# Kernel tuning notes

Measured on AMD Instinct MI355X. Metric: run time of the kernel, lower is better.

## Reference

```python
import jax, jax.numpy as jnp
import numpy as np

IMG = 1024
P0, P1 = 32, 16          # patch_size = [32, 16], P0 = 2*P1 required by stride-2 conv
C = 1                    # num_channels (must be 1 for unflatten(encoded, 1) to be valid)
N0 = (IMG // P0) ** 2    # 1024 patches at coarse scale
N1 = (IMG // P1) ** 2    # 4096 patches at fine scale
D0 = C * P0 * P0         # 1024 projection dim (coarse)
D1 = C * P1 * P1         # 256 projection dim (fine)
B = 8
BN_EPS = 1e-3            # keras BatchNormalization default
LRELU_ALPHA = 0.3        # keras LeakyReLU default


def setup_inputs() -> dict:
    key = jax.random.key(0)
    ks = jax.random.split(key, 9)
    return {
        "X": jax.random.normal(ks[0], (B, IMG, IMG, C), jnp.float32),
        "W_emb": jax.random.normal(ks[1], (N0, D0), jnp.float32) * 0.02,
        "conv_w": jax.random.normal(ks[2], (3, 3, N0, N1), jnp.float32) * 0.02,
        "conv_b": jnp.zeros((N1,), jnp.float32),
        "bn_gamma": jax.random.uniform(ks[3], (N1,), jnp.float32) + 0.5,
        "bn_beta": jax.random.normal(ks[4], (N1,), jnp.float32) * 0.1,
        "bn_mean": jax.random.normal(ks[5], (N1,), jnp.float32) * 0.1,
        "bn_var": jax.random.uniform(ks[6], (N1,), jnp.float32) + 0.5,
        "W_dense": jax.random.normal(ks[7], (D0, D0), jnp.float32) * 0.02,
        "b_dense": jnp.zeros((D0,), jnp.float32),
    }


def _patches(x, p):
    # [B,H,W,C] -> [B, (H/p)*(W/p), p, p, C]; row-major patch order, matching tf split/stack path.
    b, h, w, c = x.shape
    x = x.reshape(b, h // p, p, w // p, p, c).transpose(0, 1, 3, 2, 4, 5)
    return x.reshape(b, (h // p) * (w // p), p, p, c)


def _unpatch(x):
    # [B, n, p, p, C] -> [B, e*p, e*p, C] with e = sqrt(n); exact inverse of _patches.
    b, n, p, _, c = x.shape
    e = int(np.sqrt(n))
    x = x.reshape(b, e, e, p, p, c).transpose(0, 1, 3, 2, 4, 5)
    return x.reshape(b, e * p, e * p, c)


def reference(X, W_emb, conv_w, conv_b, bn_gamma, bn_beta, bn_mean, bn_var, W_dense, b_dense):
    b = X.shape[0]
    # fine-scale patches, flattened
    flat = _patches(X, P1).reshape(b, N1, D1)

    # positional embedding 1: positions = arange(N0) -> full embedding table
    pos1 = W_emb  # [N0, D0]

    # positional embedding 2: unflatten -> conv branch (inference: dropout = identity, BN uses moving stats)
    pe = pos1.reshape(1, N0, P0, P0, C).transpose(0, 4, 2, 3, 1).reshape(C, P0, P0, N0)  # [C,P0,P0,N0]
    y = jax.lax.conv_general_dilated(
        pe, conv_w, window_strides=(2, 2), padding='SAME',
        dimension_numbers=('NHWC', 'HWIO', 'NHWC')) + conv_b            # [C, P1, P1, N1]
    y = (y - bn_mean) * (bn_gamma / jnp.sqrt(bn_var + BN_EPS)) + bn_beta
    y = jnp.where(y > 0, y, LRELU_ALPHA * y)
    pos2 = y.reshape(1, C, P1, P1, N1).transpose(0, 4, 2, 3, 1).reshape(1, N1, D1)

    enc = flat + pos2                                                    # [B, N1, D1]
    # unflatten(.,1) -> unpatch -> repatch at coarse scale (pure reshape/transpose)
    img = _unpatch(enc.reshape(b, N1, P1, P1, 1))                        # [B, IMG, IMG, 1]
    enc = _patches(img, P0).reshape(b, N0, D0) + pos1                    # [B, N0, D0]
    return enc @ W_dense + b_dense
```

## Files before the change

kernel.cpp:

```cpp
#include <hip/hip_runtime.h>

typedef __attribute__((ext_vector_type(8))) short short8;
typedef __attribute__((ext_vector_type(4))) short short4v;
typedef __attribute__((ext_vector_type(4))) float float4v;

typedef const void __attribute__((address_space(1)))* gptr_t;
typedef void __attribute__((address_space(3)))* lptr_t;

__device__ __forceinline__ void gload_lds16(const void* g, void* l) {
    __builtin_amdgcn_global_load_lds((gptr_t)g, (lptr_t)l, 16, 0, 0);
}

__device__ __forceinline__ unsigned short f2bf(float f) {
    union { float f; unsigned int u; } v; v.f = f;
    unsigned int r = v.u + 0x7fffu + ((v.u >> 16) & 1u);
    return (unsigned short)(r >> 16);
}

__device__ __forceinline__ short8 frag_ld(const unsigned char* base, int row, int k2) {
    return *(const short8*)(base + row * 128 + (k2 ^ ((row & 7) << 4)));
}

__device__ __forceinline__ int swzB(int n) {
    return ((n ^ (n >> 3)) & 7) << 4;
}

__device__ __forceinline__ short8 frag_ldB(const unsigned char* base, int n, int k2) {
    return *(const short8*)(base + n * 128 + (k2 ^ swzB(n)));
}

__device__ __forceinline__ float4v mfma_bf16(short8 a, short8 b, float4v c) {
    return __builtin_amdgcn_mfma_f32_16x16x32_bf16(a, b, c, 0, 0, 0);
}

__global__ __launch_bounds__(256) void k_transpose_bf16(
        const float* __restrict__ in, unsigned short* __restrict__ out) {
    __shared__ float tile[32][33];
    int tx = threadIdx.x, ty = threadIdx.y;
    int x = blockIdx.x * 32 + tx;
    int ybase = blockIdx.y * 32;
#pragma unroll
    for (int j = 0; j < 4; j++)
        tile[ty + j * 8][tx] = in[(size_t)(ybase + ty + j * 8) * 1024 + x];
    __syncthreads();
    int ox = ybase + tx;
    int oybase = blockIdx.x * 32;
#pragma unroll
    for (int j = 0; j < 4; j++)
        out[(size_t)(oybase + ty + j * 8) * 1024 + ox] = f2bf(tile[tx][ty + j * 8]);
}

__global__ __launch_bounds__(256) void k_conv_gemm(
        const float* __restrict__ convw,
        const unsigned short* __restrict__ peT,
        const unsigned short* __restrict__ zerobuf,
        float* __restrict__ y_acc)
{
    __shared__ __align__(16) unsigned char ldsA[2][16384];
    __shared__ __align__(16) unsigned char ldsB[2][8192];

    const int t = threadIdx.x;
    const int L = blockIdx.x;
    const int ell = (L & 7) * 144 + (L >> 3);
    const int mt = ell & 1;
    const int nt = (ell >> 1) & 63;
    const int s  = ell >> 7;
    const int kh = s / 3, kw = s - kh * 3;
    const int ncol0 = nt * 64;

    const int l = t & 63, w = t >> 6;
    const int wm = w >> 1, wn = w & 1;
    const int l15 = l & 15;
    const int lk2 = (l >> 4) * 16;

    float4v acc[4][2] = {};

    const unsigned short* asrc[4];
    int aok[4];
#pragma unroll
    for (int i = 0; i < 4; i++) {
        int idx = i * 256 + t;
        int r = idx >> 3, c8 = idx & 7;
        int m = mt * 128 + r;
        int oh = m >> 4, ow = m & 15;
        int ih = 2 * oh + kh, iw = 2 * ow + kw;
        bool ok = (ih < 32) && (iw < 32);
        asrc[i] = ok ? (peT + (size_t)(ih * 32 + iw) * 1024 + ((c8 ^ (r & 7)) * 8))
                     : zerobuf;
        aok[i] = ok ? ~0 : 0;
    }

    const int g = t >> 4, l16v = t & 15;
    const int bk0 = g * 4;
    const int bn0 = l16v * 4;
    const float* bbase = convw + ((size_t)s * 1024 + bk0) * 4096 + ncol0 + bn0;

    float4v rb[2][4];

#pragma unroll
    for (int i = 0; i < 4; i++)
        gload_lds16(asrc[i], &ldsA[0][(i * 256 + t) * 16]);
#pragma unroll
    for (int i = 0; i < 4; i++)
        rb[0][i] = *(const float4v*)(bbase + (size_t)i * 4096);
    __builtin_amdgcn_sched_barrier(0);
#pragma unroll
    for (int i = 0; i < 4; i++)
        gload_lds16(asrc[i] + (64 & aok[i]), &ldsA[1][(i * 256 + t) * 16]);
#pragma unroll
    for (int i = 0; i < 4; i++)
        rb[1][i] = *(const float4v*)(bbase + (size_t)(64 + i) * 4096);
    asm volatile("s_waitcnt vmcnt(8)" ::: "memory");
    __builtin_amdgcn_sched_barrier(0);
#pragma unroll
    for (int i = 0; i < 4; i++) {
        int n = bn0 + i;
        short4v v;
        v.x = (short)f2bf(rb[0][0][i]);
        v.y = (short)f2bf(rb[0][1][i]);
        v.z = (short)f2bf(rb[0][2][i]);
        v.w = (short)f2bf(rb[0][3][i]);
        *(short4v*)(&ldsB[0][n * 128 + ((bk0 * 2) ^ swzB(n))]) = v;
    }
    asm volatile("s_waitcnt lgkmcnt(0)" ::: "memory");
    __builtin_amdgcn_s_barrier();

#pragma unroll
    for (int tt = 0; tt < 16; ++tt) {
        const int cur = tt & 1;

        short8 af[4][2], bfr[2][2];
#pragma unroll
        for (int mf = 0; mf < 4; mf++)
#pragma unroll
            for (int ks = 0; ks < 2; ks++)
                af[mf][ks] = frag_ld(ldsA[cur], wm * 64 + mf * 16 + l15, ks * 64 + lk2);
#pragma unroll
        for (int nf = 0; nf < 2; nf++)
#pragma unroll
            for (int ks = 0; ks < 2; ks++)
                bfr[nf][ks] = frag_ldB(ldsB[cur], wn * 32 + nf * 16 + l15, ks * 64 + lk2);
        asm volatile("s_waitcnt lgkmcnt(0)" ::: "memory");
        __builtin_amdgcn_sched_barrier(0);
        __builtin_amdgcn_s_barrier();

        if (tt < 14) {
            const int k0n = (tt + 2) * 64;
#pragma unroll
            for (int i = 0; i < 4; i++)
                gload_lds16(asrc[i] + (k0n & aok[i]), &ldsA[cur][(i * 256 + t) * 16]);
#pragma unroll
            for (int i = 0; i < 4; i++)
                rb[cur][i] = *(const float4v*)(bbase + (size_t)(k0n + i) * 4096);
        }

        __builtin_amdgcn_s_setprio(1);
#pragma unroll
        for (int mf = 0; mf < 4; mf++)
#pragma unroll
            for (int nf = 0; nf < 2; nf++)
#pragma unroll
                for (int ks = 0; ks < 2; ks++)
                    acc[mf][nf] = mfma_bf16(af[mf][ks], bfr[nf][ks], acc[mf][nf]);
        __builtin_amdgcn_s_setprio(0);

        if (tt < 15) {
            if (tt < 14) asm volatile("s_waitcnt vmcnt(8)" ::: "memory");
            else         asm volatile("s_waitcnt vmcnt(0)" ::: "memory");
            __builtin_amdgcn_sched_barrier(0);
#pragma unroll
            for (int i = 0; i < 4; i++) {
                int n = bn0 + i;
                short4v v;
                v.x = (short)f2bf(rb[cur ^ 1][0][i]);
                v.y = (short)f2bf(rb[cur ^ 1][1][i]);
                v.z = (short)f2bf(rb[cur ^ 1][2][i]);
                v.w = (short)f2bf(rb[cur ^ 1][3][i]);
                *(short4v*)(&ldsB[cur ^ 1][n * 128 + ((bk0 * 2) ^ swzB(n))]) = v;
            }
            asm volatile("s_waitcnt lgkmcnt(0)" ::: "memory");
            __builtin_amdgcn_sched_barrier(0);
            __builtin_amdgcn_s_barrier();
        }
    }

#pragma unroll
    for (int mf = 0; mf < 4; mf++) {
        int row = mt * 128 + wm * 64 + mf * 16 + (l >> 4) * 4;
#pragma unroll
        for (int nf = 0; nf < 2; nf++) {
            int col = ncol0 + wn * 32 + nf * 16 + l15;
#pragma unroll
            for (int r = 0; r < 4; r++)
                atomicAdd(&y_acc[(size_t)(row + r) * 4096 + col], acc[mf][nf][r]);
        }
    }
}

__global__ __launch_bounds__(256) void k_bn_pos2(
        const float* __restrict__ y_acc, const float* __restrict__ cb,
        const float* __restrict__ gamma, const float* __restrict__ beta,
        const float* __restrict__ mean, const float* __restrict__ var,
        float* __restrict__ pos2img) {
    int idx = blockIdx.x * 256 + threadIdx.x;
    int m = idx >> 12, oc = idx & 4095;
    float v = y_acc[idx] + cb[oc];
    v = (v - mean[oc]) * (gamma[oc] * rsqrtf(var[oc] + 1e-3f)) + beta[oc];
    v = v > 0.0f ? v : 0.3f * v;
    int y = ((oc >> 6) << 4) + (m >> 4);
    int x = ((oc & 63) << 4) + (m & 15);
    pos2img[y * 1024 + x] = v;
}

__global__ __launch_bounds__(256) void k_build_A(
        const float* __restrict__ X, const float* __restrict__ pos2img,
        const float* __restrict__ W_emb, unsigned short* __restrict__ Aenc) {
    int row = blockIdx.x;
    int n0 = row & 1023;
    int b  = row >> 10;
    int d0 = threadIdx.x * 4;
    int y = ((n0 >> 5) << 5) + (d0 >> 5);
    int x = ((n0 & 31) << 5) + (d0 & 31);
    size_t pix = (size_t)y * 1024 + x;
    float4v xv = *(const float4v*)(X + (size_t)b * 1048576 + pix);
    float4v pv = *(const float4v*)(pos2img + pix);
    float4v wv = *(const float4v*)(W_emb + (size_t)n0 * 1024 + d0);
    short4v o;
    o.x = (short)f2bf(xv.x + pv.x + wv.x);
    o.y = (short)f2bf(xv.y + pv.y + wv.y);
    o.z = (short)f2bf(xv.z + pv.z + wv.z);
    o.w = (short)f2bf(xv.w + pv.w + wv.w);
    *(short4v*)(Aenc + (size_t)row * 1024 + d0) = o;
}

__global__ __launch_bounds__(256) void k_final_gemm(
        const unsigned short* __restrict__ A,
        const unsigned short* __restrict__ Bt,
        const float* __restrict__ bias,
        float* __restrict__ C) {
    __shared__ __align__(16) unsigned char ldsA[16384];
    __shared__ __align__(16) unsigned char ldsB[16384];
    const int t = threadIdx.x;
    const int L = blockIdx.x;
    const int ell = (L & 7) * 64 + (L >> 3);
    const int col0 = (ell & 7) * 128;
    const int row0 = (ell >> 3) * 128;
    const int l = t & 63, w = t >> 6;
    const int wm = w >> 1, wn = w & 1;
    const int l15 = l & 15;
    const int lk2 = (l >> 4) * 16;

    float4v acc[4][4] = {};

    const unsigned short* asrc[4];
    const unsigned short* bsrc[4];
#pragma unroll
    for (int i = 0; i < 4; i++) {
        int idx = i * 256 + t;
        int r = idx >> 3, c8 = idx & 7;
        int cofs = (c8 ^ (r & 7)) * 8;
        asrc[i] = A  + (size_t)(row0 + r) * 1024 + cofs;
        bsrc[i] = Bt + (size_t)(col0 + r) * 1024 + cofs;
    }

    for (int k0 = 0; k0 < 1024; k0 += 64) {
#pragma unroll
        for (int i = 0; i < 4; i++) {
            int idx = i * 256 + t;
            gload_lds16(asrc[i] + k0, ldsA + idx * 16);
            gload_lds16(bsrc[i] + k0, ldsB + idx * 16);
        }
        __syncthreads();

        short8 af[4][2], bfr[4][2];
#pragma unroll
        for (int mf = 0; mf < 4; mf++)
#pragma unroll
            for (int ks = 0; ks < 2; ks++)
                af[mf][ks] = frag_ld(ldsA, wm * 64 + mf * 16 + l15, ks * 64 + lk2);
#pragma unroll
        for (int nf = 0; nf < 4; nf++)
#pragma unroll
            for (int ks = 0; ks < 2; ks++)
                bfr[nf][ks] = frag_ld(ldsB, wn * 64 + nf * 16 + l15, ks * 64 + lk2);
#pragma unroll
        for (int mf = 0; mf < 4; mf++)
#pragma unroll
            for (int nf = 0; nf < 4; nf++)
#pragma unroll
                for (int ks = 0; ks < 2; ks++)
                    acc[mf][nf] = mfma_bf16(af[mf][ks], bfr[nf][ks], acc[mf][nf]);
        __syncthreads();
    }

#pragma unroll
    for (int nf = 0; nf < 4; nf++) {
        int col = col0 + wn * 64 + nf * 16 + l15;
        float bv = bias[col];
#pragma unroll
        for (int mf = 0; mf < 4; mf++) {
            int row = row0 + wm * 64 + mf * 16 + (l >> 4) * 4;
#pragma unroll
            for (int r = 0; r < 4; r++)
                C[(size_t)(row + r) * 1024 + col] = acc[mf][nf][r] + bv;
        }
    }
}

extern "C" void kernel_launch(void* const* d_in, const int* in_sizes, int n_in,
                              void* d_out, int out_size, void* d_ws, size_t ws_size,
                              hipStream_t stream) {
    (void)in_sizes; (void)n_in; (void)out_size; (void)ws_size;
    const float* X       = (const float*)d_in[0];
    const float* W_emb   = (const float*)d_in[1];
    const float* conv_w  = (const float*)d_in[2];
    const float* conv_b  = (const float*)d_in[3];
    const float* gamma   = (const float*)d_in[4];
    const float* beta    = (const float*)d_in[5];
    const float* mean    = (const float*)d_in[6];
    const float* var     = (const float*)d_in[7];
    const float* W_dense = (const float*)d_in[8];
    const float* b_dense = (const float*)d_in[9];
    float* out = (float*)d_out;

    unsigned char* ws = (unsigned char*)d_ws;
    float*          y_acc   = (float*)(ws);
    unsigned short* zerobuf = (unsigned short*)(ws + (4u << 20));
    unsigned short* peT     = (unsigned short*)(ws + (8u << 20));
    unsigned short* WdT     = (unsigned short*)(ws + (10u << 20));
    float*          pos2img = (float*)(ws + (12u << 20));
    unsigned short* Aenc    = (unsigned short*)(ws + (16u << 20));

    hipMemsetAsync(y_acc, 0, (4u << 20) + 4096, stream);

    dim3 tb(32, 8);
    k_transpose_bf16<<<dim3(32, 32), tb, 0, stream>>>(W_emb, peT);
    k_transpose_bf16<<<dim3(32, 32), tb, 0, stream>>>(W_dense, WdT);
    k_conv_gemm<<<1152, 256, 0, stream>>>(conv_w, peT, zerobuf, y_acc);
    k_bn_pos2<<<4096, 256, 0, stream>>>(y_acc, conv_b, gamma, beta, mean, var, pos2img);
    k_build_A<<<8192, 256, 0, stream>>>(X, pos2img, W_emb, Aenc);
    k_final_gemm<<<512, 256, 0, stream>>>(Aenc, WdT, b_dense, out);
}
```

Before: 108.5 us.

## Replace conv atomics with per-tap partial buffers and full-M tiles

The conv GEMM now gives each block all 256 output rows (M) instead of half, so each conv_w tile is loaded and converted once rather than twice. Blocks write per-tap partial sums to nine separate buffers with plain stores, replacing float atomicAdd, and the BN kernel sums the nine partials. This also removes the hipMemset; the zero buffer is now written by the transpose kernel. In exchange the workspace needs 36 MB of partials, BN reads nine times more data, only 576 blocks are launched, and LDS use per block doubles.

```diff
diff --git a/kernel.cpp b/kernel.cpp
--- a/kernel.cpp
+++ b/kernel.cpp
@@ -34,9 +34,11 @@
 }
 
 __global__ __launch_bounds__(256) void k_transpose_bf16(
-        const float* __restrict__ in, unsigned short* __restrict__ out) {
+        const float* __restrict__ in, unsigned short* __restrict__ out,
+        float* __restrict__ zb) {
     __shared__ float tile[32][33];
     int tx = threadIdx.x, ty = threadIdx.y;
+    if (blockIdx.x == 0 && blockIdx.y == 0 && ty == 0) zb[tx] = 0.0f;
     int x = blockIdx.x * 32 + tx;
     int ybase = blockIdx.y * 32;
 #pragma unroll
@@ -50,39 +52,35 @@
         out[(size_t)(oybase + ty + j * 8) * 1024 + ox] = f2bf(tile[tx][ty + j * 8]);
 }
 
-__global__ __launch_bounds__(256) void k_conv_gemm(
+__global__ __launch_bounds__(256, 2) void k_conv_gemm(
         const float* __restrict__ convw,
         const unsigned short* __restrict__ peT,
         const unsigned short* __restrict__ zerobuf,
-        float* __restrict__ y_acc)
+        float* __restrict__ y_part)
 {
-    __shared__ __align__(16) unsigned char ldsA[2][16384];
+    __shared__ __align__(16) unsigned char ldsA[2][32768];
     __shared__ __align__(16) unsigned char ldsB[2][8192];
 
     const int t = threadIdx.x;
     const int L = blockIdx.x;
-    const int ell = (L & 7) * 144 + (L >> 3);
-    const int mt = ell & 1;
-    const int nt = (ell >> 1) & 63;
-    const int s  = ell >> 7;
+    const int nt = L & 63;
+    const int s  = L >> 6;
     const int kh = s / 3, kw = s - kh * 3;
     const int ncol0 = nt * 64;
 
     const int l = t & 63, w = t >> 6;
-    const int wm = w >> 1, wn = w & 1;
     const int l15 = l & 15;
     const int lk2 = (l >> 4) * 16;
 
-    float4v acc[4][2] = {};
-
-    const unsigned short* asrc[4];
-    int aok[4];
-#pragma unroll
-    for (int i = 0; i < 4; i++) {
+    float4v acc[4][4] = {};
+
+    const unsigned short* asrc[8];
+    int aok[8];
+#pragma unroll
+    for (int i = 0; i < 8; i++) {
         int idx = i * 256 + t;
         int r = idx >> 3, c8 = idx & 7;
-        int m = mt * 128 + r;
-        int oh = m >> 4, ow = m & 15;
+        int oh = r >> 4, ow = r & 15;
         int ih = 2 * oh + kh, iw = 2 * ow + kw;
         bool ok = (ih < 32) && (iw < 32);
         asrc[i] = ok ? (peT + (size_t)(ih * 32 + iw) * 1024 + ((c8 ^ (r & 7)) * 8))
@@ -98,19 +96,19 @@
     float4v rb[2][4];
 
 #pragma unroll
-    for (int i = 0; i < 4; i++)
+    for (int i = 0; i < 8; i++)
         gload_lds16(asrc[i], &ldsA[0][(i * 256 + t) * 16]);
 #pragma unroll
     for (int i = 0; i < 4; i++)
         rb[0][i] = *(const float4v*)(bbase + (size_t)i * 4096);
     __builtin_amdgcn_sched_barrier(0);
 #pragma unroll
-    for (int i = 0; i < 4; i++)
+    for (int i = 0; i < 8; i++)
         gload_lds16(asrc[i] + (64 & aok[i]), &ldsA[1][(i * 256 + t) * 16]);
 #pragma unroll
     for (int i = 0; i < 4; i++)
         rb[1][i] = *(const float4v*)(bbase + (size_t)(64 + i) * 4096);
-    asm volatile("s_waitcnt vmcnt(8)" ::: "memory");
+    asm volatile("s_waitcnt vmcnt(12)" ::: "memory");
     __builtin_amdgcn_sched_barrier(0);
 #pragma unroll
     for (int i = 0; i < 4; i++) {
@@ -129,25 +127,26 @@
     for (int tt = 0; tt < 16; ++tt) {
         const int cur = tt & 1;
 
-        short8 af[4][2], bfr[2][2];
+        short8 af[4][2], bfr[4][2];
 #pragma unroll
         for (int mf = 0; mf < 4; mf++)
 #pragma unroll
             for (int ks = 0; ks < 2; ks++)
-                af[mf][ks] = frag_ld(ldsA[cur], wm * 64 + mf * 16 + l15, ks * 64 + lk2);
-#pragma unroll
-        for (int nf = 0; nf < 2; nf++)
+                af[mf][ks] = frag_ld(ldsA[cur], w * 64 + mf * 16 + l15, ks * 64 + lk2);
+#pragma unroll
+        for (int nf = 0; nf < 4; nf++)
 #pragma unroll
             for (int ks = 0; ks < 2; ks++)
-                bfr[nf][ks] = frag_ldB(ldsB[cur], wn * 32 + nf * 16 + l15, ks * 64 + lk2);
+                bfr[nf][ks] = frag_ldB(ldsB[cur], nf * 16 + l15, ks * 64 + lk2);
         asm volatile("s_waitcnt lgkmcnt(0)" ::: "memory");
         __builtin_amdgcn_sched_barrier(0);
         __builtin_amdgcn_s_barrier();
+        __builtin_amdgcn_sched_barrier(0);
 
         if (tt < 14) {
             const int k0n = (tt + 2) * 64;
 #pragma unroll
-            for (int i = 0; i < 4; i++)
+            for (int i = 0; i < 8; i++)
                 gload_lds16(asrc[i] + (k0n & aok[i]), &ldsA[cur][(i * 256 + t) * 16]);
 #pragma unroll
             for (int i = 0; i < 4; i++)
@@ -158,14 +157,14 @@
 #pragma unroll
         for (int mf = 0; mf < 4; mf++)
 #pragma unroll
-            for (int nf = 0; nf < 2; nf++)
+            for (int nf = 0; nf < 4; nf++)
 #pragma unroll
                 for (int ks = 0; ks < 2; ks++)
                     acc[mf][nf] = mfma_bf16(af[mf][ks], bfr[nf][ks], acc[mf][nf]);
         __builtin_amdgcn_s_setprio(0);
 
         if (tt < 15) {
-            if (tt < 14) asm volatile("s_waitcnt vmcnt(8)" ::: "memory");
+            if (tt < 14) asm volatile("s_waitcnt vmcnt(12)" ::: "memory");
             else         asm volatile("s_waitcnt vmcnt(0)" ::: "memory");
             __builtin_amdgcn_sched_barrier(0);
 #pragma unroll
@@ -184,27 +183,31 @@
         }
     }
 
+    float* yp = y_part + (size_t)s * 1048576;
 #pragma unroll
     for (int mf = 0; mf < 4; mf++) {
-        int row = mt * 128 + wm * 64 + mf * 16 + (l >> 4) * 4;
-#pragma unroll
-        for (int nf = 0; nf < 2; nf++) {
-            int col = ncol0 + wn * 32 + nf * 16 + l15;
-#pragma unroll
-            for (int r = 0; r < 4; r++)
-                atomicAdd(&y_acc[(size_t)(row + r) * 4096 + col], acc[mf][nf][r]);
+        int row = w * 64 + mf * 16 + (l >> 4) * 4;
+#pragma unroll
+        for (int nf = 0; nf < 4; nf++) {
+            int col = ncol0 + nf * 16 + l15;
+#pragma unroll
+            for (int rr = 0; rr < 4; rr++)
+                yp[(size_t)(row + rr) * 4096 + col] = acc[mf][nf][rr];
         }
     }
 }
 
 __global__ __launch_bounds__(256) void k_bn_pos2(
-        const float* __restrict__ y_acc, const float* __restrict__ cb,
+        const float* __restrict__ y_part, const float* __restrict__ cb,
         const float* __restrict__ gamma, const float* __restrict__ beta,
         const float* __restrict__ mean, const float* __restrict__ var,
         float* __restrict__ pos2img) {
     int idx = blockIdx.x * 256 + threadIdx.x;
     int m = idx >> 12, oc = idx & 4095;
-    float v = y_acc[idx] + cb[oc];
+    float v = cb[oc];
+#pragma unroll
+    for (int s = 0; s < 9; s++)
+        v += y_part[(size_t)s * 1048576 + idx];
     v = (v - mean[oc]) * (gamma[oc] * rsqrtf(var[oc] + 1e-3f)) + beta[oc];
     v = v > 0.0f ? v : 0.3f * v;
     int y = ((oc >> 6) << 4) + (m >> 4);
@@ -324,20 +327,18 @@
     float* out = (float*)d_out;
 
     unsigned char* ws = (unsigned char*)d_ws;
-    float*          y_acc   = (float*)(ws);
-    unsigned short* zerobuf = (unsigned short*)(ws + (4u << 20));
-    unsigned short* peT     = (unsigned short*)(ws + (8u << 20));
-    unsigned short* WdT     = (unsigned short*)(ws + (10u << 20));
-    float*          pos2img = (float*)(ws + (12u << 20));
-    unsigned short* Aenc    = (unsigned short*)(ws + (16u << 20));
-
-    hipMemsetAsync(y_acc, 0, (4u << 20) + 4096, stream);
+    float*          y_part  = (float*)(ws);
+    float*          zerobuf = (float*)(ws + (36u << 20));
+    unsigned short* peT     = (unsigned short*)(ws + (38u << 20));
+    unsigned short* WdT     = (unsigned short*)(ws + (40u << 20));
+    float*          pos2img = (float*)(ws + (42u << 20));
+    unsigned short* Aenc    = (unsigned short*)(ws + (48u << 20));
 
     dim3 tb(32, 8);
-    k_transpose_bf16<<<dim3(32, 32), tb, 0, stream>>>(W_emb, peT);
-    k_transpose_bf16<<<dim3(32, 32), tb, 0, stream>>>(W_dense, WdT);
-    k_conv_gemm<<<1152, 256, 0, stream>>>(conv_w, peT, zerobuf, y_acc);
-    k_bn_pos2<<<4096, 256, 0, stream>>>(y_acc, conv_b, gamma, beta, mean, var, pos2img);
+    k_transpose_bf16<<<dim3(32, 32), tb, 0, stream>>>(W_emb, peT, zerobuf);
+    k_transpose_bf16<<<dim3(32, 32), tb, 0, stream>>>(W_dense, WdT, zerobuf);
+    k_conv_gemm<<<576, 256, 0, stream>>>(conv_w, peT, (const unsigned short*)zerobuf, y_part);
+    k_bn_pos2<<<4096, 256, 0, stream>>>(y_part, conv_b, gamma, beta, mean, var, pos2img);
     k_build_A<<<8192, 256, 0, stream>>>(X, pos2img, W_emb, Aenc);
     k_final_gemm<<<512, 256, 0, stream>>>(Aenc, WdT, b_dense, out);
 }
```

After: 112.9 us. 4.0% more time.

## Replace conv atomics with per-tap partial buffers and deepen B prefetch

Applied to the files above, without the earlier changes.

The conv GEMM no longer atomically adds into a zeroed accumulator. Each of the 9 kernel taps writes its own partial slab, and the BN kernel sums the nine slabs, which removes the memset and the atomic contention. The zero buffer is now cleared inside the transpose kernel. The fp32 weight loads use a three-deep register ring buffer, prefetching one stage further ahead, and the kernel gains a launch-bounds occupancy hint. The cost is 36 MB of extra partial writes and reads in the BN kernel, plus higher register pressure.

```diff
diff --git a/kernel.cpp b/kernel.cpp
--- a/kernel.cpp
+++ b/kernel.cpp
@@ -34,9 +34,11 @@
 }
 
 __global__ __launch_bounds__(256) void k_transpose_bf16(
-        const float* __restrict__ in, unsigned short* __restrict__ out) {
+        const float* __restrict__ in, unsigned short* __restrict__ out,
+        float* __restrict__ zb) {
     __shared__ float tile[32][33];
     int tx = threadIdx.x, ty = threadIdx.y;
+    if (blockIdx.x == 0 && blockIdx.y == 0 && ty == 0) zb[tx] = 0.0f;
     int x = blockIdx.x * 32 + tx;
     int ybase = blockIdx.y * 32;
 #pragma unroll
@@ -50,11 +52,11 @@
         out[(size_t)(oybase + ty + j * 8) * 1024 + ox] = f2bf(tile[tx][ty + j * 8]);
 }
 
-__global__ __launch_bounds__(256) void k_conv_gemm(
+__global__ __launch_bounds__(256, 3) void k_conv_gemm(
         const float* __restrict__ convw,
         const unsigned short* __restrict__ peT,
         const unsigned short* __restrict__ zerobuf,
-        float* __restrict__ y_acc)
+        float* __restrict__ y_part)
 {
     __shared__ __align__(16) unsigned char ldsA[2][16384];
     __shared__ __align__(16) unsigned char ldsB[2][8192];
@@ -95,7 +97,7 @@
     const int bn0 = l16v * 4;
     const float* bbase = convw + ((size_t)s * 1024 + bk0) * 4096 + ncol0 + bn0;
 
-    float4v rb[2][4];
+    float4v rb[3][4];
 
 #pragma unroll
     for (int i = 0; i < 4; i++)
@@ -110,7 +112,11 @@
 #pragma unroll
     for (int i = 0; i < 4; i++)
         rb[1][i] = *(const float4v*)(bbase + (size_t)(64 + i) * 4096);
-    asm volatile("s_waitcnt vmcnt(8)" ::: "memory");
+    __builtin_amdgcn_sched_barrier(0);
+#pragma unroll
+    for (int i = 0; i < 4; i++)
+        rb[2][i] = *(const float4v*)(bbase + (size_t)(128 + i) * 4096);
+    asm volatile("s_waitcnt vmcnt(16)" ::: "memory");
     __builtin_amdgcn_sched_barrier(0);
 #pragma unroll
     for (int i = 0; i < 4; i++) {
@@ -143,15 +149,19 @@
         asm volatile("s_waitcnt lgkmcnt(0)" ::: "memory");
         __builtin_amdgcn_sched_barrier(0);
         __builtin_amdgcn_s_barrier();
+        __builtin_amdgcn_sched_barrier(0);
 
         if (tt < 14) {
             const int k0n = (tt + 2) * 64;
 #pragma unroll
             for (int i = 0; i < 4; i++)
                 gload_lds16(asrc[i] + (k0n & aok[i]), &ldsA[cur][(i * 256 + t) * 16]);
+        }
+        if (tt < 13) {
+            const int k0b = (tt + 3) * 64;
 #pragma unroll
             for (int i = 0; i < 4; i++)
-                rb[cur][i] = *(const float4v*)(bbase + (size_t)(k0n + i) * 4096);
+                rb[tt % 3][i] = *(const float4v*)(bbase + (size_t)(k0b + i) * 4096);
         }
 
         __builtin_amdgcn_s_setprio(1);
@@ -165,17 +175,18 @@
         __builtin_amdgcn_s_setprio(0);
 
         if (tt < 15) {
-            if (tt < 14) asm volatile("s_waitcnt vmcnt(8)" ::: "memory");
-            else         asm volatile("s_waitcnt vmcnt(0)" ::: "memory");
+            if (tt <= 12)      asm volatile("s_waitcnt vmcnt(16)" ::: "memory");
+            else if (tt == 13) asm volatile("s_waitcnt vmcnt(12)" ::: "memory");
+            else               asm volatile("s_waitcnt vmcnt(0)" ::: "memory");
             __builtin_amdgcn_sched_barrier(0);
 #pragma unroll
             for (int i = 0; i < 4; i++) {
                 int n = bn0 + i;
                 short4v v;
-                v.x = (short)f2bf(rb[cur ^ 1][0][i]);
-                v.y = (short)f2bf(rb[cur ^ 1][1][i]);
-                v.z = (short)f2bf(rb[cur ^ 1][2][i]);
-                v.w = (short)f2bf(rb[cur ^ 1][3][i]);
+                v.x = (short)f2bf(rb[(tt + 1) % 3][0][i]);
+                v.y = (short)f2bf(rb[(tt + 1) % 3][1][i]);
+                v.z = (short)f2bf(rb[(tt + 1) % 3][2][i]);
+                v.w = (short)f2bf(rb[(tt + 1) % 3][3][i]);
                 *(short4v*)(&ldsB[cur ^ 1][n * 128 + ((bk0 * 2) ^ swzB(n))]) = v;
             }
             asm volatile("s_waitcnt lgkmcnt(0)" ::: "memory");
@@ -184,6 +195,7 @@
         }
     }
 
+    float* yp = y_part + (size_t)s * 1048576;
 #pragma unroll
     for (int mf = 0; mf < 4; mf++) {
         int row = mt * 128 + wm * 64 + mf * 16 + (l >> 4) * 4;
@@ -191,20 +203,23 @@
         for (int nf = 0; nf < 2; nf++) {
             int col = ncol0 + wn * 32 + nf * 16 + l15;
 #pragma unroll
-            for (int r = 0; r < 4; r++)
-                atomicAdd(&y_acc[(size_t)(row + r) * 4096 + col], acc[mf][nf][r]);
+            for (int rr = 0; rr < 4; rr++)
+                yp[(size_t)(row + rr) * 4096 + col] = acc[mf][nf][rr];
         }
     }
 }
 
 __global__ __launch_bounds__(256) void k_bn_pos2(
-        const float* __restrict__ y_acc, const float* __restrict__ cb,
+        const float* __restrict__ y_part, const float* __restrict__ cb,
         const float* __restrict__ gamma, const float* __restrict__ beta,
         const float* __restrict__ mean, const float* __restrict__ var,
         float* __restrict__ pos2img) {
     int idx = blockIdx.x * 256 + threadIdx.x;
     int m = idx >> 12, oc = idx & 4095;
-    float v = y_acc[idx] + cb[oc];
+    float v = cb[oc];
+#pragma unroll
+    for (int s = 0; s < 9; s++)
+        v += y_part[(size_t)s * 1048576 + idx];
     v = (v - mean[oc]) * (gamma[oc] * rsqrtf(var[oc] + 1e-3f)) + beta[oc];
     v = v > 0.0f ? v : 0.3f * v;
     int y = ((oc >> 6) << 4) + (m >> 4);
@@ -324,20 +339,18 @@
     float* out = (float*)d_out;
 
     unsigned char* ws = (unsigned char*)d_ws;
-    float*          y_acc   = (float*)(ws);
-    unsigned short* zerobuf = (unsigned short*)(ws + (4u << 20));
-    unsigned short* peT     = (unsigned short*)(ws + (8u << 20));
-    unsigned short* WdT     = (unsigned short*)(ws + (10u << 20));
-    float*          pos2img = (float*)(ws + (12u << 20));
-    unsigned short* Aenc    = (unsigned short*)(ws + (16u << 20));
-
-    hipMemsetAsync(y_acc, 0, (4u << 20) + 4096, stream);
+    float*          y_part  = (float*)(ws);
+    float*          zerobuf = (float*)(ws + (36u << 20));
+    unsigned short* peT     = (unsigned short*)(ws + (38u << 20));
+    unsigned short* WdT     = (unsigned short*)(ws + (40u << 20));
+    float*          pos2img = (float*)(ws + (42u << 20));
+    unsigned short* Aenc    = (unsigned short*)(ws + (48u << 20));
 
     dim3 tb(32, 8);
-    k_transpose_bf16<<<dim3(32, 32), tb, 0, stream>>>(W_emb, peT);
-    k_transpose_bf16<<<dim3(32, 32), tb, 0, stream>>>(W_dense, WdT);
-    k_conv_gemm<<<1152, 256, 0, stream>>>(conv_w, peT, zerobuf, y_acc);
-    k_bn_pos2<<<4096, 256, 0, stream>>>(y_acc, conv_b, gamma, beta, mean, var, pos2img);
+    k_transpose_bf16<<<dim3(32, 32), tb, 0, stream>>>(W_emb, peT, zerobuf);
+    k_transpose_bf16<<<dim3(32, 32), tb, 0, stream>>>(W_dense, WdT, zerobuf);
+    k_conv_gemm<<<1152, 256, 0, stream>>>(conv_w, peT, (const unsigned short*)zerobuf, y_part);
+    k_bn_pos2<<<4096, 256, 0, stream>>>(y_part, conv_b, gamma, beta, mean, var, pos2img);
     k_build_A<<<8192, 256, 0, stream>>>(X, pos2img, W_emb, Aenc);
     k_final_gemm<<<512, 256, 0, stream>>>(Aenc, WdT, b_dense, out);
 }
```

Measured after the change: 122.4 us. 1.13x slower.
